# Kernel optimization log

Hardware: AMD Instinct MI355X
Metric: run time of the kernel (lower is better)

The kernel has to match this reference:

```python
import jax, jax.numpy as jnp
import numpy as np

C = 64
CQ = C // 8


def setup_inputs() -> dict:
    key = jax.random.key(0)
    ks = jax.random.split(key, 8)
    x = jax.random.normal(ks[0], (8, C, 64, 64), dtype=jnp.float32)
    s = 1.0 / np.sqrt(C)
    Wq = jax.random.normal(ks[1], (CQ, C), dtype=jnp.float32) * s
    bq = jax.random.normal(ks[2], (CQ,), dtype=jnp.float32) * s
    Wk = jax.random.normal(ks[3], (CQ, C), dtype=jnp.float32) * s
    bk = jax.random.normal(ks[4], (CQ,), dtype=jnp.float32) * s
    Wv = jax.random.normal(ks[5], (C, C), dtype=jnp.float32) * s
    bv = jax.random.normal(ks[6], (C,), dtype=jnp.float32) * s
    gamma = jnp.array([0.5], dtype=jnp.float32)  # nonzero so value path contributes
    return {"x": x, "Wq": Wq, "bq": bq, "Wk": Wk, "bk": bk, "Wv": Wv, "bv": bv, "gamma": gamma}


def reference(x, Wq, bq, Wk, bk, Wv, bv, gamma):
    B, Cc, H, W = x.shape
    xf = x.reshape(B, Cc, H * W)  # [B, C, N]
    # 1x1 conv == channel-mixing linear
    f = jnp.einsum('oc,bcn->bon', Wq, xf) + bq[None, :, None]  # [B, C/8, N]
    g = jnp.einsum('oc,bcn->bon', Wk, xf) + bk[None, :, None]  # [B, C/8, N]
    h = jnp.einsum('oc,bcn->bon', Wv, xf) + bv[None, :, None]  # [B, C, N]
    # scores[b,i,j] = f[b,:,i] . g[b,:,j]; softmax over dim=1 (query dim i)
    scores = jnp.einsum('bdi,bdj->bij', f, g)  # [B, N, N]
    beta = jax.nn.softmax(scores, axis=1)
    o = gamma[0] * jnp.einsum('bcn,bnm->bcm', h, beta) + xf
    return o.reshape(B, Cc, H, W)
```

## Files before the change

kernel.cpp:

```cpp
#include <hip/hip_runtime.h>
#include <hip/hip_fp16.h>


typedef _Float16 half8_t __attribute__((ext_vector_type(8)));
typedef _Float16 half4_t __attribute__((ext_vector_type(4)));
typedef _Float16 half2_t __attribute__((ext_vector_type(2)));
typedef __fp16  fp16x2  __attribute__((ext_vector_type(2)));
typedef float float4_t __attribute__((ext_vector_type(4)));

#define NTOK 4096
#define PRH 72
#define LOG2E 1.44269504088896340736f

#if __has_builtin(__builtin_amdgcn_exp2f)
__device__ __forceinline__ float fexp2(float x) { return __builtin_amdgcn_exp2f(x); }
#else
__device__ __forceinline__ float fexp2(float x) { return exp2f(x); }
#endif

__device__ __forceinline__ half2_t pkcvt(float a, float b) {
    fp16x2 v = __builtin_amdgcn_cvt_pkrtz(a, b);
    return __builtin_bit_cast(half2_t, v);
}

__global__ __launch_bounds__(320) void proj_kernel(
    const float* __restrict__ x,
    const float* __restrict__ Wq, const float* __restrict__ bq,
    const float* __restrict__ Wk, const float* __restrict__ bk,
    const float* __restrict__ Wv, const float* __restrict__ bv,
    __half* __restrict__ fTR, __half* __restrict__ gT16, __half* __restrict__ hM)
{
    __shared__ __align__(16) _Float16 xh[64 * PRH];
    const int t  = threadIdx.x;
    const int kt = blockIdx.x;
    const int b  = blockIdx.y;
    const int n0 = kt * 64;

    if (t < 256) {
#pragma unroll
        for (int i = 0; i < 4; i++) {
            const int idx = t + i * 256;
            const int c = idx >> 4, f4 = idx & 15;
            float4 v = *(const float4*)(x + (((size_t)(b * 64 + c)) << 12) + n0 + f4 * 4);
            xh[(f4 * 4 + 0) * PRH + c] = (_Float16)v.x;
            xh[(f4 * 4 + 1) * PRH + c] = (_Float16)v.y;
            xh[(f4 * 4 + 2) * PRH + c] = (_Float16)v.z;
            xh[(f4 * 4 + 3) * PRH + c] = (_Float16)v.w;
        }
    }

    const int w    = t >> 6;
    const int lane = t & 63;
    const int q    = lane >> 4;
    const int ml   = lane & 15;

    const float* wrow;
    if (w == 0) wrow = (ml < 8) ? (Wq + ml * 64) : (Wk + (ml - 8) * 64);
    else        wrow = Wv + ((w - 1) * 16 + ml) * 64;
    half4_t afr[4];
#pragma unroll
    for (int ks = 0; ks < 4; ks++) {
        float4 wv4 = *(const float4*)(wrow + ks * 16 + q * 4);
        afr[ks] = (half4_t){(_Float16)wv4.x, (_Float16)wv4.y,
                            (_Float16)wv4.z, (_Float16)wv4.w};
    }
    float4 bias4;
    if (w == 0) bias4 = (q < 2) ? *(const float4*)(bq + q * 4)
                                : *(const float4*)(bk + (q - 2) * 4);
    else        bias4 = *(const float4*)(bv + (w - 1) * 16 + q * 4);

    __syncthreads();

#pragma unroll
    for (int cg = 0; cg < 4; cg++) {
        float4_t acc = (float4_t){0.f, 0.f, 0.f, 0.f};
#pragma unroll
        for (int ks = 0; ks < 4; ks++) {
            half4_t bfr = *(const half4_t*)(&xh[(cg * 16 + ml) * PRH + ks * 16 + q * 4]);
            acc = __builtin_amdgcn_mfma_f32_16x16x16f16(afr[ks], bfr, acc, 0, 0, 0);
        }
        acc[0] += bias4.x; acc[1] += bias4.y; acc[2] += bias4.z; acc[3] += bias4.w;
        const int tok = n0 + cg * 16 + ml;

        if (w == 0) {
            if (q < 2) {
                half4_t fv = {(_Float16)(acc[0] * LOG2E), (_Float16)(acc[1] * LOG2E),
                              (_Float16)(acc[2] * LOG2E), (_Float16)(acc[3] * LOG2E)};
                *(half4_t*)(fTR + ((size_t)b << 15) +
                            (size_t)(kt * 16 + ml) * 32 + q * 16 + cg * 4) = fv;
            }
            float gn2p = acc[0] * acc[0] + acc[1] * acc[1] +
                         acc[2] * acc[2] + acc[3] * acc[3];
            float gn2 = gn2p + __shfl_xor(gn2p, 16, 64);
            if (q >= 2) {
                half4_t gv = {(_Float16)acc[0], (_Float16)acc[1],
                              (_Float16)acc[2], (_Float16)acc[3]};
                __half* gp = gT16 + (size_t)((b << 12) + tok) * 16;
                *(half4_t*)(gp + (q - 2) * 4) = gv;
                if (q == 2) {
                    const float M = (LOG2E * 4.6f) * __builtin_sqrtf(gn2) + 1.0f;
                    *(half4_t*)(gp + 8) = (half4_t){(_Float16)(-M), 0, 0, 0};
                } else {
                    *(half4_t*)(gp + 12) = (half4_t){};
                }
            }
        } else {
            const int ch = (w - 1) * 16 + q * 4;
#pragma unroll
            for (int r = 0; r < 4; r++)
                hM[(((size_t)b * 64 + ch + r) << 12) + tok] = __float2half(acc[r]);
        }
    }
}

template<int NT>
__global__ __launch_bounds__(256) void attn_kernel(
    const __half* __restrict__ fTR, const __half* __restrict__ gT16,
    const __half* __restrict__ hM,
    __half* __restrict__ Pacc, float* __restrict__ Lsum)
{
    __shared__ __align__(16) _Float16 hl[2][64 * PRH];
    const int tid   = threadIdx.x;
    const int w     = tid >> 6;
    const int lane  = tid & 63;
    const int q     = lane >> 4;
    const int ml    = lane & 15;
    const int b     = blockIdx.y;
    const int split = blockIdx.z;
    const int colA  = blockIdx.x * 128 + w * 16 + ml;
    const int colB  = colA + 64;
    const bool qlo  = (q < 2);

    half4_t gfA = *(const half4_t*)(gT16 + ((size_t)((b << 12) + colA)) * 16 + q * 4);
    half4_t gfB = *(const half4_t*)(gT16 + ((size_t)((b << 12) + colB)) * 16 + q * 4);

    float4_t accA[4], accB[4];
#pragma unroll
    for (int cg = 0; cg < 4; cg++) {
        accA[cg] = (float4_t){0.f, 0.f, 0.f, 0.f};
        accB[cg] = (float4_t){0.f, 0.f, 0.f, 0.f};
    }
    float lsA0 = 0.f, lsA1 = 0.f, lsA2 = 0.f, lsA3 = 0.f;
    float lsB0 = 0.f, lsB1 = 0.f, lsB2 = 0.f, lsB3 = 0.f;

    const int kt0 = split * NT;
    const int c0  = tid >> 3;
    const int g0  = tid & 7;

    const __half* srow0 = hM + ((size_t)(b * 64 + c0) << 12) + kt0 * 64 + g0 * 8;
    const __half* srow1 = srow0 + ((size_t)32 << 12);
    const __half* fptr  = fTR + ((size_t)b << 15) + (size_t)(kt0 * 16 + ml) * 32 + q * 16;

    half4_t padv = (half4_t){};
    if (q == 2) padv[0] = (_Float16)1.0f;

    uint4 s0 = *(const uint4*)srow0;
    uint4 s1 = *(const uint4*)srow1;
    half4_t afn0 = padv, afn1 = padv, afn2 = padv, afn3 = padv;
    if (qlo) {
        afn0 = *(const half4_t*)(fptr);
        afn1 = *(const half4_t*)(fptr + 4);
        afn2 = *(const half4_t*)(fptr + 8);
        afn3 = *(const half4_t*)(fptr + 12);
    }
    *(uint4*)(&hl[0][c0 * PRH + g0 * 8])        = s0;
    *(uint4*)(&hl[0][(c0 + 32) * PRH + g0 * 8]) = s1;
    __syncthreads();

#pragma unroll 1
    for (int kt = 0; kt < NT; kt++) {
        const _Float16* hbL = &hl[kt & 1][ml * PRH + q * 4];

        float4_t stA0 = __builtin_amdgcn_mfma_f32_16x16x16f16(
            afn0, gfA, (float4_t){0.f, 0.f, 0.f, 0.f}, 0, 0, 0);
        float4_t stA1 = __builtin_amdgcn_mfma_f32_16x16x16f16(
            afn1, gfA, (float4_t){0.f, 0.f, 0.f, 0.f}, 0, 0, 0);
        float4_t stA2 = __builtin_amdgcn_mfma_f32_16x16x16f16(
            afn2, gfA, (float4_t){0.f, 0.f, 0.f, 0.f}, 0, 0, 0);
        float4_t stA3 = __builtin_amdgcn_mfma_f32_16x16x16f16(
            afn3, gfA, (float4_t){0.f, 0.f, 0.f, 0.f}, 0, 0, 0);
        float4_t stB0 = __builtin_amdgcn_mfma_f32_16x16x16f16(
            afn0, gfB, (float4_t){0.f, 0.f, 0.f, 0.f}, 0, 0, 0);
        float4_t stB1 = __builtin_amdgcn_mfma_f32_16x16x16f16(
            afn1, gfB, (float4_t){0.f, 0.f, 0.f, 0.f}, 0, 0, 0);
        float4_t stB2 = __builtin_amdgcn_mfma_f32_16x16x16f16(
            afn2, gfB, (float4_t){0.f, 0.f, 0.f, 0.f}, 0, 0, 0);
        float4_t stB3 = __builtin_amdgcn_mfma_f32_16x16x16f16(
            afn3, gfB, (float4_t){0.f, 0.f, 0.f, 0.f}, 0, 0, 0);

        if (kt + 1 < NT) {
            if (qlo) {
                afn0 = *(const half4_t*)(fptr + 512);
                afn1 = *(const half4_t*)(fptr + 516);
                afn2 = *(const half4_t*)(fptr + 520);
                afn3 = *(const half4_t*)(fptr + 524);
            }
            s0 = *(const uint4*)(srow0 + 64);
            s1 = *(const uint4*)(srow1 + 64);
            fptr  += 512;
            srow0 += 64;
            srow1 += 64;
        }

        {
            float pA0 = fexp2(stA0[0]), pA1 = fexp2(stA0[1]),
                  pA2 = fexp2(stA0[2]), pA3 = fexp2(stA0[3]);
            float pB0 = fexp2(stB0[0]), pB1 = fexp2(stB0[1]),
                  pB2 = fexp2(stB0[2]), pB3 = fexp2(stB0[3]);
            lsA0 += pA0; lsA1 += pA1; lsA2 += pA2; lsA3 += pA3;
            lsB0 += pB0; lsB1 += pB1; lsB2 += pB2; lsB3 += pB3;
            half2_t a_lo = pkcvt(pA0, pA1), a_hi = pkcvt(pA2, pA3);
            half2_t b_lo = pkcvt(pB0, pB1), b_hi = pkcvt(pB2, pB3);
            half4_t pfA = {a_lo[0], a_lo[1], a_hi[0], a_hi[1]};
            half4_t pfB = {b_lo[0], b_lo[1], b_hi[0], b_hi[1]};
#pragma unroll
            for (int cg = 0; cg < 4; cg++) {
                half4_t ah = *(const half4_t*)(hbL + cg * (16 * PRH) + 0 * 16);
                accA[cg] = __builtin_amdgcn_mfma_f32_16x16x16f16(ah, pfA, accA[cg], 0, 0, 0);
                accB[cg] = __builtin_amdgcn_mfma_f32_16x16x16f16(ah, pfB, accB[cg], 0, 0, 0);
            }
        }
        {
            float pA0 = fexp2(stA1[0]), pA1 = fexp2(stA1[1]),
                  pA2 = fexp2(stA1[2]), pA3 = fexp2(stA1[3]);
            float pB0 = fexp2(stB1[0]), pB1 = fexp2(stB1[1]),
                  pB2 = fexp2(stB1[2]), pB3 = fexp2(stB1[3]);
            lsA0 += pA0; lsA1 += pA1; lsA2 += pA2; lsA3 += pA3;
            lsB0 += pB0; lsB1 += pB1; lsB2 += pB2; lsB3 += pB3;
            half2_t a_lo = pkcvt(pA0, pA1), a_hi = pkcvt(pA2, pA3);
            half2_t b_lo = pkcvt(pB0, pB1), b_hi = pkcvt(pB2, pB3);
            half4_t pfA = {a_lo[0], a_lo[1], a_hi[0], a_hi[1]};
            half4_t pfB = {b_lo[0], b_lo[1], b_hi[0], b_hi[1]};
#pragma unroll
            for (int cg = 0; cg < 4; cg++) {
                half4_t ah = *(const half4_t*)(hbL + cg * (16 * PRH) + 1 * 16);
                accA[cg] = __builtin_amdgcn_mfma_f32_16x16x16f16(ah, pfA, accA[cg], 0, 0, 0);
                accB[cg] = __builtin_amdgcn_mfma_f32_16x16x16f16(ah, pfB, accB[cg], 0, 0, 0);
            }
        }
        {
            float pA0 = fexp2(stA2[0]), pA1 = fexp2(stA2[1]),
                  pA2 = fexp2(stA2[2]), pA3 = fexp2(stA2[3]);
            float pB0 = fexp2(stB2[0]), pB1 = fexp2(stB2[1]),
                  pB2 = fexp2(stB2[2]), pB3 = fexp2(stB2[3]);
            lsA0 += pA0; lsA1 += pA1; lsA2 += pA2; lsA3 += pA3;
            lsB0 += pB0; lsB1 += pB1; lsB2 += pB2; lsB3 += pB3;
            half2_t a_lo = pkcvt(pA0, pA1), a_hi = pkcvt(pA2, pA3);
            half2_t b_lo = pkcvt(pB0, pB1), b_hi = pkcvt(pB2, pB3);
            half4_t pfA = {a_lo[0], a_lo[1], a_hi[0], a_hi[1]};
            half4_t pfB = {b_lo[0], b_lo[1], b_hi[0], b_hi[1]};
#pragma unroll
            for (int cg = 0; cg < 4; cg++) {
                half4_t ah = *(const half4_t*)(hbL + cg * (16 * PRH) + 2 * 16);
                accA[cg] = __builtin_amdgcn_mfma_f32_16x16x16f16(ah, pfA, accA[cg], 0, 0, 0);
                accB[cg] = __builtin_amdgcn_mfma_f32_16x16x16f16(ah, pfB, accB[cg], 0, 0, 0);
            }
        }
        {
            float pA0 = fexp2(stA3[0]), pA1 = fexp2(stA3[1]),
                  pA2 = fexp2(stA3[2]), pA3 = fexp2(stA3[3]);
            float pB0 = fexp2(stB3[0]), pB1 = fexp2(stB3[1]),
                  pB2 = fexp2(stB3[2]), pB3 = fexp2(stB3[3]);
            lsA0 += pA0; lsA1 += pA1; lsA2 += pA2; lsA3 += pA3;
            lsB0 += pB0; lsB1 += pB1; lsB2 += pB2; lsB3 += pB3;
            half2_t a_lo = pkcvt(pA0, pA1), a_hi = pkcvt(pA2, pA3);
            half2_t b_lo = pkcvt(pB0, pB1), b_hi = pkcvt(pB2, pB3);
            half4_t pfA = {a_lo[0], a_lo[1], a_hi[0], a_hi[1]};
            half4_t pfB = {b_lo[0], b_lo[1], b_hi[0], b_hi[1]};
#pragma unroll
            for (int cg = 0; cg < 4; cg++) {
                half4_t ah = *(const half4_t*)(hbL + cg * (16 * PRH) + 3 * 16);
                accA[cg] = __builtin_amdgcn_mfma_f32_16x16x16f16(ah, pfA, accA[cg], 0, 0, 0);
                accB[cg] = __builtin_amdgcn_mfma_f32_16x16x16f16(ah, pfB, accB[cg], 0, 0, 0);
            }
        }

        if (kt + 1 < NT) {
            _Float16* hn = &hl[(kt + 1) & 1][0];
            *(uint4*)(&hn[c0 * PRH + g0 * 8])        = s0;
            *(uint4*)(&hn[(c0 + 32) * PRH + g0 * 8]) = s1;
        }
        __syncthreads();
    }

    float lA = (lsA0 + lsA1) + (lsA2 + lsA3);
    lA += __shfl_xor(lA, 16, 64);
    lA += __shfl_xor(lA, 32, 64);
    float lB = (lsB0 + lsB1) + (lsB2 + lsB3);
    lB += __shfl_xor(lB, 16, 64);
    lB += __shfl_xor(lB, 32, 64);

    __half* pa = Pacc + (((size_t)(split * 8 + b) * 64) << 12);
#pragma unroll
    for (int cg = 0; cg < 4; cg++)
#pragma unroll
        for (int r = 0; r < 4; r++) {
            int ch = cg * 16 + q * 4 + r;
            pa[((size_t)ch << 12) + colA] = __float2half(accA[cg][r]);
            pa[((size_t)ch << 12) + colB] = __float2half(accB[cg][r]);
        }
    if (q == 0) {
        Lsum[((size_t)(split * 8 + b) << 12) + colA] = lA;
        Lsum[((size_t)(split * 8 + b) << 12) + colB] = lB;
    }
}

template<int S>
__global__ __launch_bounds__(256) void merge_kernel(
    const __half* __restrict__ Pacc, const float* __restrict__ Lsum,
    const float* __restrict__ x, const float* __restrict__ gammap,
    float* __restrict__ out)
{
    __shared__ float invL[64];
    const int tid  = threadIdx.x;
    const int c4   = tid & 15;
    const int chh  = tid >> 4;
    const int b    = blockIdx.y;
    const int col0 = blockIdx.x * 64;
    const int ch   = blockIdx.z * 16 + chh;

    if (tid < 64) {
        float L = 0.f;
#pragma unroll
        for (int s = 0; s < S; s++)
            L += Lsum[((size_t)(s * 8 + b) << 12) + col0 + tid];
        invL[tid] = gammap[0] / L;
    }
    __syncthreads();

    const int cc = c4 * 4;
    const size_t base = (((size_t)b * 64 + ch) << 12) + col0 + cc;
    float4 xv = *(const float4*)(x + base);
    float o0 = 0.f, o1 = 0.f, o2 = 0.f, o3 = 0.f;
#pragma unroll
    for (int s = 0; s < S; s++) {
        half4_t pv = *(const half4_t*)(Pacc +
            (((size_t)(s * 8 + b) * 64 + ch) << 12) + col0 + cc);
        o0 += (float)pv[0];
        o1 += (float)pv[1];
        o2 += (float)pv[2];
        o3 += (float)pv[3];
    }
    float4 ov;
    ov.x = o0 * invL[cc]     + xv.x;
    ov.y = o1 * invL[cc + 1] + xv.y;
    ov.z = o2 * invL[cc + 2] + xv.z;
    ov.w = o3 * invL[cc + 3] + xv.w;
    *(float4*)(out + base) = ov;
}

extern "C" void kernel_launch(void* const* d_in, const int* in_sizes, int n_in,
                              void* d_out, int out_size, void* d_ws, size_t ws_size,
                              hipStream_t stream) {
    const float* x     = (const float*)d_in[0];
    const float* Wq    = (const float*)d_in[1];
    const float* bq    = (const float*)d_in[2];
    const float* Wk    = (const float*)d_in[3];
    const float* bk    = (const float*)d_in[4];
    const float* Wv    = (const float*)d_in[5];
    const float* bv    = (const float*)d_in[6];
    const float* gamma = (const float*)d_in[7];
    float* out = (float*)d_out;

    const size_t fr_bytes  = (size_t)8 * 32768 * 2;
    const size_t g_bytes   = (size_t)8 * NTOK * 16 * 2;
    const size_t hM_bytes  = (size_t)8 * 64 * NTOK * 2;
    const size_t pa_split  = (size_t)8 * 64 * NTOK * 2;
    const size_t l_split   = (size_t)8 * NTOK * sizeof(float);
    const size_t base_need = fr_bytes + g_bytes + hM_bytes;

    int S = 1;
    if (ws_size >= base_need + 4 * (pa_split + l_split)) S = 4;
    else if (ws_size >= base_need + 2 * (pa_split + l_split)) S = 2;

    char* p = (char*)d_ws;
    __half* fTR  = (__half*)p;  p += fr_bytes;
    __half* gT16 = (__half*)p;  p += g_bytes;
    __half* hM   = (__half*)p;  p += hM_bytes;
    __half* Pacc = (__half*)p;  p += (size_t)S * pa_split;
    float*  Lsum = (float*)p;

    proj_kernel<<<dim3(64, 8), 320, 0, stream>>>(x, Wq, bq, Wk, bk, Wv, bv,
                                                 fTR, gT16, hM);
    if (S == 4) {
        attn_kernel<16><<<dim3(32, 8, 4), 256, 0, stream>>>(fTR, gT16, hM, Pacc, Lsum);
        merge_kernel<4><<<dim3(64, 8, 4), 256, 0, stream>>>(Pacc, Lsum, x, gamma, out);
    } else if (S == 2) {
        attn_kernel<32><<<dim3(32, 8, 2), 256, 0, stream>>>(fTR, gT16, hM, Pacc, Lsum);
        merge_kernel<2><<<dim3(64, 8, 4), 256, 0, stream>>>(Pacc, Lsum, x, gamma, out);
    } else {
        attn_kernel<64><<<dim3(32, 8, 1), 256, 0, stream>>>(fTR, gT16, hM, Pacc, Lsum);
        merge_kernel<1><<<dim3(64, 8, 4), 256, 0, stream>>>(Pacc, Lsum, x, gamma, out);
    }
}
```

Measured before the change: 121.3 us.

## Compute softmax row sums via MFMA with ones, pad f records, swizzle proj LDS

The attention kernel now accumulates the softmax denominators with extra MFMA instructions that multiply a ones vector by the probability fragments, replacing scalar adds and the final cross-lane shuffles. The f records are widened to 64 halves with the padding constant pre-stored, so every lane does unconditional 16-byte loads without a per-lane branch. The projection kernel is split into 32-token blocks to launch twice as many blocks, and its LDS transpose uses an XOR swizzle to cut bank conflicts. The cost is extra MFMA work per tile and twice the memory traffic for f.

```diff
diff --git a/kernel.cpp b/kernel.cpp
--- a/kernel.cpp
+++ b/kernel.cpp
@@ -30,22 +30,25 @@
     const float* __restrict__ Wv, const float* __restrict__ bv,
     __half* __restrict__ fTR, __half* __restrict__ gT16, __half* __restrict__ hM)
 {
-    __shared__ __align__(16) _Float16 xh[64 * PRH];
-    const int t  = threadIdx.x;
-    const int kt = blockIdx.x;
-    const int b  = blockIdx.y;
-    const int n0 = kt * 64;
+    __shared__ __align__(16) _Float16 xh[32 * PRH];
+    const int t      = threadIdx.x;
+    const int blk    = blockIdx.x;
+    const int b      = blockIdx.y;
+    const int n0     = blk * 32;
+    const int kt64   = blk >> 1;
+    const int t4base = (blk & 1) * 2;
 
     if (t < 256) {
 #pragma unroll
-        for (int i = 0; i < 4; i++) {
+        for (int i = 0; i < 2; i++) {
             const int idx = t + i * 256;
-            const int c = idx >> 4, f4 = idx & 15;
+            const int c = idx >> 3, f4 = idx & 7;
             float4 v = *(const float4*)(x + (((size_t)(b * 64 + c)) << 12) + n0 + f4 * 4);
-            xh[(f4 * 4 + 0) * PRH + c] = (_Float16)v.x;
-            xh[(f4 * 4 + 1) * PRH + c] = (_Float16)v.y;
-            xh[(f4 * 4 + 2) * PRH + c] = (_Float16)v.z;
-            xh[(f4 * 4 + 3) * PRH + c] = (_Float16)v.w;
+            const int cs = c ^ ((f4 & 3) << 4);
+            xh[(f4 * 4 + 0) * PRH + cs] = (_Float16)v.x;
+            xh[(f4 * 4 + 1) * PRH + cs] = (_Float16)v.y;
+            xh[(f4 * 4 + 2) * PRH + cs] = (_Float16)v.z;
+            xh[(f4 * 4 + 3) * PRH + cs] = (_Float16)v.w;
         }
     }
 
@@ -72,22 +75,29 @@
     __syncthreads();
 
 #pragma unroll
-    for (int cg = 0; cg < 4; cg++) {
+    for (int cg = 0; cg < 2; cg++) {
+        const int tok  = cg * 16 + ml;
+        const int swz  = (tok >> 2) & 3;
         float4_t acc = (float4_t){0.f, 0.f, 0.f, 0.f};
 #pragma unroll
         for (int ks = 0; ks < 4; ks++) {
-            half4_t bfr = *(const half4_t*)(&xh[(cg * 16 + ml) * PRH + ks * 16 + q * 4]);
+            half4_t bfr = *(const half4_t*)(&xh[tok * PRH + ((ks ^ swz) * 16 + q * 4)]);
             acc = __builtin_amdgcn_mfma_f32_16x16x16f16(afr[ks], bfr, acc, 0, 0, 0);
         }
         acc[0] += bias4.x; acc[1] += bias4.y; acc[2] += bias4.z; acc[3] += bias4.w;
-        const int tok = n0 + cg * 16 + ml;
+        const int gtok = n0 + tok;
+        const int t4   = t4base + cg;
 
         if (w == 0) {
+            __half* rec = fTR + ((size_t)b << 16) + (size_t)(kt64 * 16 + ml) * 64;
             if (q < 2) {
                 half4_t fv = {(_Float16)(acc[0] * LOG2E), (_Float16)(acc[1] * LOG2E),
                               (_Float16)(acc[2] * LOG2E), (_Float16)(acc[3] * LOG2E)};
-                *(half4_t*)(fTR + ((size_t)b << 15) +
-                            (size_t)(kt * 16 + ml) * 32 + q * 16 + cg * 4) = fv;
+                *(half4_t*)(rec + q * 16 + t4 * 4) = fv;
+            } else {
+                half4_t cv = (half4_t){};
+                if (q == 2) cv[0] = (_Float16)1.0f;
+                *(half4_t*)(rec + q * 16 + t4 * 4) = cv;
             }
             float gn2p = acc[0] * acc[0] + acc[1] * acc[1] +
                          acc[2] * acc[2] + acc[3] * acc[3];
@@ -95,7 +105,7 @@
             if (q >= 2) {
                 half4_t gv = {(_Float16)acc[0], (_Float16)acc[1],
                               (_Float16)acc[2], (_Float16)acc[3]};
-                __half* gp = gT16 + (size_t)((b << 12) + tok) * 16;
+                __half* gp = gT16 + (size_t)((b << 12) + gtok) * 16;
                 *(half4_t*)(gp + (q - 2) * 4) = gv;
                 if (q == 2) {
                     const float M = (LOG2E * 4.6f) * __builtin_sqrtf(gn2) + 1.0f;
@@ -108,7 +118,7 @@
             const int ch = (w - 1) * 16 + q * 4;
 #pragma unroll
             for (int r = 0; r < 4; r++)
-                hM[(((size_t)b * 64 + ch + r) << 12) + tok] = __float2half(acc[r]);
+                hM[(((size_t)b * 64 + ch + r) << 12) + gtok] = __float2half(acc[r]);
         }
     }
 }
@@ -129,7 +139,6 @@
     const int split = blockIdx.z;
     const int colA  = blockIdx.x * 128 + w * 16 + ml;
     const int colB  = colA + 64;
-    const bool qlo  = (q < 2);
 
     half4_t gfA = *(const half4_t*)(gT16 + ((size_t)((b << 12) + colA)) * 16 + q * 4);
     half4_t gfB = *(const half4_t*)(gT16 + ((size_t)((b << 12) + colB)) * 16 + q * 4);
@@ -140,8 +149,10 @@
         accA[cg] = (float4_t){0.f, 0.f, 0.f, 0.f};
         accB[cg] = (float4_t){0.f, 0.f, 0.f, 0.f};
     }
-    float lsA0 = 0.f, lsA1 = 0.f, lsA2 = 0.f, lsA3 = 0.f;
-    float lsB0 = 0.f, lsB1 = 0.f, lsB2 = 0.f, lsB3 = 0.f;
+    float4_t accLA = (float4_t){0.f, 0.f, 0.f, 0.f};
+    float4_t accLB = (float4_t){0.f, 0.f, 0.f, 0.f};
+    const half4_t onesf = {(_Float16)1.0f, (_Float16)1.0f,
+                           (_Float16)1.0f, (_Float16)1.0f};
 
     const int kt0 = split * NT;
     const int c0  = tid >> 3;
@@ -149,20 +160,12 @@
 
     const __half* srow0 = hM + ((size_t)(b * 64 + c0) << 12) + kt0 * 64 + g0 * 8;
     const __half* srow1 = srow0 + ((size_t)32 << 12);
-    const __half* fptr  = fTR + ((size_t)b << 15) + (size_t)(kt0 * 16 + ml) * 32 + q * 16;
-
-    half4_t padv = (half4_t){};
-    if (q == 2) padv[0] = (_Float16)1.0f;
+    const __half* fptr  = fTR + ((size_t)b << 16) + (size_t)(kt0 * 16 + ml) * 64 + q * 16;
 
     uint4 s0 = *(const uint4*)srow0;
     uint4 s1 = *(const uint4*)srow1;
-    half4_t afn0 = padv, afn1 = padv, afn2 = padv, afn3 = padv;
-    if (qlo) {
-        afn0 = *(const half4_t*)(fptr);
-        afn1 = *(const half4_t*)(fptr + 4);
-        afn2 = *(const half4_t*)(fptr + 8);
-        afn3 = *(const half4_t*)(fptr + 12);
-    }
+    half8_t f01 = *(const half8_t*)fptr;
+    half8_t f23 = *(const half8_t*)(fptr + 8);
     *(uint4*)(&hl[0][c0 * PRH + g0 * 8])        = s0;
     *(uint4*)(&hl[0][(c0 + 32) * PRH + g0 * 8]) = s1;
     __syncthreads();
@@ -170,6 +173,10 @@
 #pragma unroll 1
     for (int kt = 0; kt < NT; kt++) {
         const _Float16* hbL = &hl[kt & 1][ml * PRH + q * 4];
+        half4_t afn0 = __builtin_shufflevector(f01, f01, 0, 1, 2, 3);
+        half4_t afn1 = __builtin_shufflevector(f01, f01, 4, 5, 6, 7);
+        half4_t afn2 = __builtin_shufflevector(f23, f23, 0, 1, 2, 3);
+        half4_t afn3 = __builtin_shufflevector(f23, f23, 4, 5, 6, 7);
 
         float4_t stA0 = __builtin_amdgcn_mfma_f32_16x16x16f16(
             afn0, gfA, (float4_t){0.f, 0.f, 0.f, 0.f}, 0, 0, 0);
@@ -189,15 +196,11 @@
             afn3, gfB, (float4_t){0.f, 0.f, 0.f, 0.f}, 0, 0, 0);
 
         if (kt + 1 < NT) {
-            if (qlo) {
-                afn0 = *(const half4_t*)(fptr + 512);
-                afn1 = *(const half4_t*)(fptr + 516);
-                afn2 = *(const half4_t*)(fptr + 520);
-                afn3 = *(const half4_t*)(fptr + 524);
-            }
+            f01 = *(const half8_t*)(fptr + 1024);
+            f23 = *(const half8_t*)(fptr + 1032);
             s0 = *(const uint4*)(srow0 + 64);
             s1 = *(const uint4*)(srow1 + 64);
-            fptr  += 512;
+            fptr  += 1024;
             srow0 += 64;
             srow1 += 64;
         }
@@ -207,12 +210,12 @@
                   pA2 = fexp2(stA0[2]), pA3 = fexp2(stA0[3]);
             float pB0 = fexp2(stB0[0]), pB1 = fexp2(stB0[1]),
                   pB2 = fexp2(stB0[2]), pB3 = fexp2(stB0[3]);
-            lsA0 += pA0; lsA1 += pA1; lsA2 += pA2; lsA3 += pA3;
-            lsB0 += pB0; lsB1 += pB1; lsB2 += pB2; lsB3 += pB3;
             half2_t a_lo = pkcvt(pA0, pA1), a_hi = pkcvt(pA2, pA3);
             half2_t b_lo = pkcvt(pB0, pB1), b_hi = pkcvt(pB2, pB3);
             half4_t pfA = {a_lo[0], a_lo[1], a_hi[0], a_hi[1]};
             half4_t pfB = {b_lo[0], b_lo[1], b_hi[0], b_hi[1]};
+            accLA = __builtin_amdgcn_mfma_f32_16x16x16f16(onesf, pfA, accLA, 0, 0, 0);
+            accLB = __builtin_amdgcn_mfma_f32_16x16x16f16(onesf, pfB, accLB, 0, 0, 0);
 #pragma unroll
             for (int cg = 0; cg < 4; cg++) {
                 half4_t ah = *(const half4_t*)(hbL + cg * (16 * PRH) + 0 * 16);
@@ -225,12 +228,12 @@
                   pA2 = fexp2(stA1[2]), pA3 = fexp2(stA1[3]);
             float pB0 = fexp2(stB1[0]), pB1 = fexp2(stB1[1]),
                   pB2 = fexp2(stB1[2]), pB3 = fexp2(stB1[3]);
-            lsA0 += pA0; lsA1 += pA1; lsA2 += pA2; lsA3 += pA3;
-            lsB0 += pB0; lsB1 += pB1; lsB2 += pB2; lsB3 += pB3;
             half2_t a_lo = pkcvt(pA0, pA1), a_hi = pkcvt(pA2, pA3);
             half2_t b_lo = pkcvt(pB0, pB1), b_hi = pkcvt(pB2, pB3);
             half4_t pfA = {a_lo[0], a_lo[1], a_hi[0], a_hi[1]};
             half4_t pfB = {b_lo[0], b_lo[1], b_hi[0], b_hi[1]};
+            accLA = __builtin_amdgcn_mfma_f32_16x16x16f16(onesf, pfA, accLA, 0, 0, 0);
+            accLB = __builtin_amdgcn_mfma_f32_16x16x16f16(onesf, pfB, accLB, 0, 0, 0);
 #pragma unroll
             for (int cg = 0; cg < 4; cg++) {
                 half4_t ah = *(const half4_t*)(hbL + cg * (16 * PRH) + 1 * 16);
@@ -243,12 +246,12 @@
                   pA2 = fexp2(stA2[2]), pA3 = fexp2(stA2[3]);
             float pB0 = fexp2(stB2[0]), pB1 = fexp2(stB2[1]),
                   pB2 = fexp2(stB2[2]), pB3 = fexp2(stB2[3]);
-            lsA0 += pA0; lsA1 += pA1; lsA2 += pA2; lsA3 += pA3;
-            lsB0 += pB0; lsB1 += pB1; lsB2 += pB2; lsB3 += pB3;
             half2_t a_lo = pkcvt(pA0, pA1), a_hi = pkcvt(pA2, pA3);
             half2_t b_lo = pkcvt(pB0, pB1), b_hi = pkcvt(pB2, pB3);
             half4_t pfA = {a_lo[0], a_lo[1], a_hi[0], a_hi[1]};
             half4_t pfB = {b_lo[0], b_lo[1], b_hi[0], b_hi[1]};
+            accLA = __builtin_amdgcn_mfma_f32_16x16x16f16(onesf, pfA, accLA, 0, 0, 0);
+            accLB = __builtin_amdgcn_mfma_f32_16x16x16f16(onesf, pfB, accLB, 0, 0, 0);
 #pragma unroll
             for (int cg = 0; cg < 4; cg++) {
                 half4_t ah = *(const half4_t*)(hbL + cg * (16 * PRH) + 2 * 16);
@@ -261,12 +264,12 @@
                   pA2 = fexp2(stA3[2]), pA3 = fexp2(stA3[3]);
             float pB0 = fexp2(stB3[0]), pB1 = fexp2(stB3[1]),
                   pB2 = fexp2(stB3[2]), pB3 = fexp2(stB3[3]);
-            lsA0 += pA0; lsA1 += pA1; lsA2 += pA2; lsA3 += pA3;
-            lsB0 += pB0; lsB1 += pB1; lsB2 += pB2; lsB3 += pB3;
             half2_t a_lo = pkcvt(pA0, pA1), a_hi = pkcvt(pA2, pA3);
             half2_t b_lo = pkcvt(pB0, pB1), b_hi = pkcvt(pB2, pB3);
             half4_t pfA = {a_lo[0], a_lo[1], a_hi[0], a_hi[1]};
             half4_t pfB = {b_lo[0], b_lo[1], b_hi[0], b_hi[1]};
+            accLA = __builtin_amdgcn_mfma_f32_16x16x16f16(onesf, pfA, accLA, 0, 0, 0);
+            accLB = __builtin_amdgcn_mfma_f32_16x16x16f16(onesf, pfB, accLB, 0, 0, 0);
 #pragma unroll
             for (int cg = 0; cg < 4; cg++) {
                 half4_t ah = *(const half4_t*)(hbL + cg * (16 * PRH) + 3 * 16);
@@ -283,13 +286,6 @@
         __syncthreads();
     }
 
-    float lA = (lsA0 + lsA1) + (lsA2 + lsA3);
-    lA += __shfl_xor(lA, 16, 64);
-    lA += __shfl_xor(lA, 32, 64);
-    float lB = (lsB0 + lsB1) + (lsB2 + lsB3);
-    lB += __shfl_xor(lB, 16, 64);
-    lB += __shfl_xor(lB, 32, 64);
-
     __half* pa = Pacc + (((size_t)(split * 8 + b) * 64) << 12);
 #pragma unroll
     for (int cg = 0; cg < 4; cg++)
@@ -300,8 +296,8 @@
             pa[((size_t)ch << 12) + colB] = __float2half(accB[cg][r]);
         }
     if (q == 0) {
-        Lsum[((size_t)(split * 8 + b) << 12) + colA] = lA;
-        Lsum[((size_t)(split * 8 + b) << 12) + colB] = lB;
+        Lsum[((size_t)(split * 8 + b) << 12) + colA] = accLA[0];
+        Lsum[((size_t)(split * 8 + b) << 12) + colB] = accLB[0];
     }
 }
 
@@ -362,7 +358,7 @@
     const float* gamma = (const float*)d_in[7];
     float* out = (float*)d_out;
 
-    const size_t fr_bytes  = (size_t)8 * 32768 * 2;
+    const size_t fr_bytes  = (size_t)8 * 65536 * 2;
     const size_t g_bytes   = (size_t)8 * NTOK * 16 * 2;
     const size_t hM_bytes  = (size_t)8 * 64 * NTOK * 2;
     const size_t pa_split  = (size_t)8 * 64 * NTOK * 2;
@@ -380,8 +376,8 @@
     __half* Pacc = (__half*)p;  p += (size_t)S * pa_split;
     float*  Lsum = (float*)p;
 
-    proj_kernel<<<dim3(64, 8), 320, 0, stream>>>(x, Wq, bq, Wk, bk, Wv, bv,
-                                                 fTR, gT16, hM);
+    proj_kernel<<<dim3(128, 8), 320, 0, stream>>>(x, Wq, bq, Wk, bk, Wv, bv,
+                                                  fTR, gT16, hM);
     if (S == 4) {
         attn_kernel<16><<<dim3(32, 8, 4), 256, 0, stream>>>(fTR, gT16, hM, Pacc, Lsum);
         merge_kernel<4><<<dim3(64, 8, 4), 256, 0, stream>>>(Pacc, Lsum, x, gamma, out);
```

Measured after the change: 121.1 us. No clear change (-0.2%).
